# Kernel optimization log

Hardware: AMD Instinct MI355X
Metric: run time of the kernel (lower is better)

## Reference

```python
import jax, jax.numpy as jnp
import numpy as np

B, L, D, H = 8, 1024, 512, 8  # L must equal len_ for the skew trick
DH = D // H


def setup_inputs() -> dict:
    key = jax.random.key(0)
    ks = jax.random.split(key, 6)
    s = 0.02
    return {
        "x": jax.random.normal(ks[0], (B, L, D), dtype=jnp.float32),
        "Wq": jax.random.normal(ks[1], (D, D), dtype=jnp.float32) * s,
        "Wk": jax.random.normal(ks[2], (D, D), dtype=jnp.float32) * s,
        "Wv": jax.random.normal(ks[3], (D, D), dtype=jnp.float32) * s,
        "We": jax.random.normal(ks[4], (L, DH), dtype=jnp.float32) * s,  # e_projection weight: (len_, d_head)
        "Wo": jax.random.normal(ks[5], (D, D), dtype=jnp.float32) * s,
        "bo": jnp.zeros((D,), dtype=jnp.float32),
        "unused": 0,
    }


def reference(x, Wq, Wk, Wv, We, Wo, bo, unused):
    Bx, Lx, Dx = x.shape
    q = (x @ Wq.T).reshape(Bx, Lx, H, DH)  # blhd
    k = (x @ Wk.T).reshape(Bx, Lx, H, DH)
    v = (x @ Wv.T).reshape(Bx, Lx, H, DH)

    # relative-position logits: e_projection(q) then permute -> (B, H, L, len_)
    qe = jnp.einsum('blhd,ed->bhle', q, We)

    # 'skew' trick: reflect-pad right by L-1, zero-pad (right 1, bottom L-1),
    # reshape (B,H,2L-1,2L) -> (B,H,2L,2L-1), slice [:L, L-1:] -> (B,H,L,L)
    qe = jnp.pad(qe, ((0, 0), (0, 0), (0, 0), (0, Lx - 1)), mode='reflect')
    qe = jnp.pad(qe, ((0, 0), (0, 0), (0, Lx - 1), (0, 1)))
    qe = qe.reshape(Bx, H, 2 * Lx, 2 * Lx - 1)
    s_rel = qe[:, :, :Lx, Lx - 1:]

    scale = 1.0 / jnp.sqrt(jnp.asarray(DH, dtype=x.dtype))
    scores = jnp.einsum('blhd,bshd->bhls', q, k)
    A = jax.nn.softmax(scale * (scores + s_rel), axis=-1)
    V = jnp.einsum('bhls,bshd->blhd', A, v).reshape(Bx, Lx, Dx)
    return V @ Wo.T + bo
```

## Files before the change

### kernel.cpp

```cpp
#include <hip/hip_runtime.h>

#define Lc 1024
#define Dc 512
#define Hc 8
#define DHc 64

typedef __attribute__((ext_vector_type(8))) short bf16x8;
typedef __attribute__((ext_vector_type(4))) float f32x4;

typedef __attribute__((address_space(1))) const unsigned int guint;
typedef __attribute__((address_space(3))) unsigned int luint;

__device__ __forceinline__ void gload_lds16(const void* g, void* l) {
    __builtin_amdgcn_global_load_lds((guint*)g, (luint*)l, 16, 0, 0);
}

__device__ __forceinline__ unsigned short f2bf(float f) {
    unsigned u = __float_as_uint(f);
    u += 0x7fffu + ((u >> 16) & 1u);
    return (unsigned short)(u >> 16);
}
__device__ __forceinline__ unsigned pk2(float a, float b) {
    return (unsigned)f2bf(a) | ((unsigned)f2bf(b) << 16);
}
__device__ __forceinline__ unsigned pk2t(float a, float b) {
    return __builtin_amdgcn_perm(__float_as_uint(b), __float_as_uint(a), 0x07060302u);
}
__device__ __forceinline__ float bf2f(unsigned short s) { return __uint_as_float(((unsigned)s) << 16); }

__global__ void cvt_all_kernel(
    const float* __restrict__ x,  const float* __restrict__ Wq,
    const float* __restrict__ Wk, const float* __restrict__ Wv,
    const float* __restrict__ Wo, const float* __restrict__ We,
    unsigned short* __restrict__ xb,  unsigned short* __restrict__ wqb,
    unsigned short* __restrict__ wkb, unsigned short* __restrict__ wvb,
    unsigned short* __restrict__ wob, unsigned short* __restrict__ wet)
{
    int bid = blockIdx.x;
    const float* src; unsigned short* dst; size_t base;
    if      (bid < 4096) { src = x;  dst = xb;  base = (size_t)bid * 1024; }
    else if (bid < 4352) { src = Wq; dst = wqb; base = (size_t)(bid-4096) * 1024; }
    else if (bid < 4608) { src = Wk; dst = wkb; base = (size_t)(bid-4352) * 1024; }
    else if (bid < 4864) { src = Wv; dst = wvb; base = (size_t)(bid-4608) * 1024; }
    else if (bid < 5120) { src = Wo; dst = wob; base = (size_t)(bid-4864) * 1024; }
    else                 { src = We; dst = wet; base = (size_t)(bid-5120) * 1024; }
    size_t i = base + (size_t)threadIdx.x * 4;
    float4 a = *(const float4*)&src[i];
    *(uint2*)&dst[i] = make_uint2(pk2(a.x, a.y), pk2(a.z, a.w));
}

__global__ __launch_bounds__(256, 3) void proj_mfma_kernel(
    const unsigned short* __restrict__ xb,
    const unsigned short* __restrict__ wq, const unsigned short* __restrict__ wk,
    const unsigned short* __restrict__ wv,
    unsigned short* __restrict__ qo, unsigned short* __restrict__ ko,
    unsigned short* __restrict__ vtg, float qscale)
{
    const unsigned short* W;
    if (blockIdx.z == 0)      W = wq;
    else if (blockIdx.z == 1) W = wk;
    else                      W = wv;

    __shared__ unsigned short smem[128 * 136];
    unsigned short* As = smem;
    unsigned short* Bs = smem + 8192;

    const int t = threadIdx.x;
    const int lane = t & 63, w = t >> 6;
    const int lq = lane >> 4, ln = lane & 15;
    const int m0 = blockIdx.y * 128, n0 = blockIdx.x * 128;
    const int wm = (w & 1) * 64, wn = (w >> 1) * 64;
    const int srow = t >> 3;
    const int lsg  = ((t & 7) ^ ((t >> 3) & 7)) * 8;
    const int key  = ln & 7;

    f32x4 acc[4][4];
    #pragma unroll
    for (int i = 0; i < 4; i++)
        #pragma unroll
        for (int j = 0; j < 4; j++) acc[i][j] = (f32x4){0.f,0.f,0.f,0.f};

    for (int c0 = 0; c0 < 512; c0 += 64) {
        __syncthreads();
        #pragma unroll
        for (int g = 0; g < 4; g++) {
            gload_lds16(&xb[(size_t)(m0 + 32*g + srow) * 512 + c0 + lsg], &As[(32*g + srow)*64 + (t&7)*8]);
            gload_lds16(&W [(size_t)(n0 + 32*g + srow) * 512 + c0 + lsg], &Bs[(32*g + srow)*64 + (t&7)*8]);
        }
        __syncthreads();

        #pragma unroll
        for (int kk = 0; kk < 2; kk++) {
            bf16x8 af[4], bf[4];
            #pragma unroll
            for (int i = 0; i < 4; i++)
                af[i] = *(bf16x8*)&As[(wm + 16*i + ln)*64 + ((kk*4 + lq) ^ key)*8];
            #pragma unroll
            for (int j = 0; j < 4; j++)
                bf[j] = *(bf16x8*)&Bs[(wn + 16*j + ln)*64 + ((kk*4 + lq) ^ key)*8];
            #pragma unroll
            for (int i = 0; i < 4; i++)
                #pragma unroll
                for (int j = 0; j < 4; j++)
                    acc[i][j] = __builtin_amdgcn_mfma_f32_16x16x32_bf16(af[i], bf[j], acc[i][j], 0, 0, 0);
        }
    }

    if (blockIdx.z < 2) {
        unsigned short* out = (blockIdx.z == 0) ? qo : ko;
        const float osc = (blockIdx.z == 0) ? qscale : 1.0f;
        #pragma unroll
        for (int i = 0; i < 4; i++) {
            #pragma unroll
            for (int r = 0; r < 4; r++) {
                int m = m0 + wm + 16*i + 4*lq + r;
                int b = m >> 10, l = m & 1023;
                #pragma unroll
                for (int j = 0; j < 4; j++) {
                    int n = n0 + wn + 16*j + ln;
                    int h = n >> 6, dh = n & 63;
                    out[((size_t)((b*Hc + h)*Lc + l))*DHc + dh] = f2bf(acc[i][j][r] * osc);
                }
            }
        }
    } else {
        __syncthreads();
        unsigned short* Ts = smem;
        #pragma unroll
        for (int i = 0; i < 4; i++) {
            int mlb = wm + 16*i + 4*lq;
            #pragma unroll
            for (int j = 0; j < 4; j++) {
                int nl = wn + 16*j + ln;
                *(uint2*)&Ts[nl*136 + mlb] = make_uint2(pk2(acc[i][j][0], acc[i][j][1]),
                                                        pk2(acc[i][j][2], acc[i][j][3]));
            }
        }
        __syncthreads();
        const int b = m0 >> 10, l0m = m0 & 1023;
        const int nl = t >> 1, seg = (t & 1) * 64;
        const int ng = n0 + nl, h = ng >> 6, dh = ng & 63;
        unsigned short* dst = vtg + (((size_t)(b*Hc + h))*DHc + dh)*Lc + l0m + seg;
        #pragma unroll
        for (int u = 0; u < 8; u++)
            *(uint4*)&dst[8*u] = *(uint4*)&Ts[nl*136 + seg + 8*u];
    }
}

__global__ __launch_bounds__(256, 4) void out_mfma_kernel(
    const unsigned short* __restrict__ A, const unsigned short* __restrict__ W,
    const float* __restrict__ bias, float* __restrict__ out)
{
    __shared__ unsigned short As[64 * 64];
    __shared__ unsigned short Bs[64 * 64];

    const int t = threadIdx.x;
    const int lane = t & 63, w = t >> 6;
    const int lq = lane >> 4, ln = lane & 15;
    const int m0 = blockIdx.y * 64, n0 = blockIdx.x * 64;
    const int wm = (w & 1) * 32, wn = (w >> 1) * 32;
    const int srow = t >> 3;
    const int lsg  = ((t & 7) ^ ((t >> 3) & 7)) * 8;
    const int key  = ln & 7;

    f32x4 acc[2][2];
    #pragma unroll
    for (int i = 0; i < 2; i++)
        #pragma unroll
        for (int j = 0; j < 2; j++) acc[i][j] = (f32x4){0.f,0.f,0.f,0.f};

    for (int c0 = 0; c0 < 512; c0 += 64) {
        __syncthreads();
        #pragma unroll
        for (int g = 0; g < 2; g++) {
            gload_lds16(&A[(size_t)(m0 + 32*g + srow) * 512 + c0 + lsg], &As[(32*g + srow)*64 + (t&7)*8]);
            gload_lds16(&W[(size_t)(n0 + 32*g + srow) * 512 + c0 + lsg], &Bs[(32*g + srow)*64 + (t&7)*8]);
        }
        __syncthreads();

        #pragma unroll
        for (int kk = 0; kk < 2; kk++) {
            bf16x8 af[2], bf[2];
            #pragma unroll
            for (int i = 0; i < 2; i++)
                af[i] = *(bf16x8*)&As[(wm + 16*i + ln)*64 + ((kk*4 + lq) ^ key)*8];
            #pragma unroll
            for (int j = 0; j < 2; j++)
                bf[j] = *(bf16x8*)&Bs[(wn + 16*j + ln)*64 + ((kk*4 + lq) ^ key)*8];
            #pragma unroll
            for (int i = 0; i < 2; i++)
                #pragma unroll
                for (int j = 0; j < 2; j++)
                    acc[i][j] = __builtin_amdgcn_mfma_f32_16x16x32_bf16(af[i], bf[j], acc[i][j], 0, 0, 0);
        }
    }

    float bb[2];
    #pragma unroll
    for (int j = 0; j < 2; j++) bb[j] = bias[n0 + wn + 16*j + ln];

    #pragma unroll
    for (int i = 0; i < 2; i++) {
        #pragma unroll
        for (int r = 0; r < 4; r++) {
            int m = m0 + wm + 16*i + 4*lq + r;
            #pragma unroll
            for (int j = 0; j < 2; j++) {
                int n = n0 + wn + 16*j + ln;
                out[(size_t)m * Dc + n] = acc[i][j][r] + bb[j];
            }
        }
    }
}

__global__ __launch_bounds__(256, 4) void attn_v9_kernel(
    const unsigned short* __restrict__ q, const unsigned short* __restrict__ k,
    const unsigned short* __restrict__ vtg, const unsigned short* __restrict__ wet,
    unsigned short* __restrict__ attn)
{
    __shared__ unsigned short ksp [2 * 64 * 32];
    __shared__ unsigned short vtp [2 * 64 * 32];
    __shared__ unsigned short ps2 [64 * 64];
    __shared__ unsigned short qes [128 * 64];

    unsigned short* wesp = ps2;

    const int t    = threadIdx.x;
    const int lane = t & 63, w = t >> 6;
    const int lq   = lane >> 4, ln = lane & 15;
    const int si   = w >> 1;
    const int li   = w & 1;

    const int n   = blockIdx.x;
    const int xcd = n & 7, idx = n >> 3;
    const int bh  = xcd * 8 + (idx >> 4);
    const int l0  = (idx & 15) * 64;

    const unsigned short* qb  = q   + (size_t)bh * (Lc * DHc);
    const unsigned short* kb  = k   + (size_t)bh * (Lc * DHc);
    const unsigned short* vtb = vtg + (size_t)bh * (DHc * Lc);

    const int trow = t >> 2;
    const int sseg = ((t & 3) ^ ((t >> 4) & 3)) * 8;
    const int swz  = (ln >> 2) & 3;

    const bf16x8 onesf = {(short)0x3F80,(short)0x3F80,(short)0x3F80,(short)0x3F80,
                          (short)0x3F80,(short)0x3F80,(short)0x3F80,(short)0x3F80};

    bf16x8 qf[2][2];
    #pragma unroll
    for (int lt = 0; lt < 2; lt++)
        #pragma unroll
        for (int kk = 0; kk < 2; kk++)
            qf[lt][kk] = *(const bf16x8*)&qb[(size_t)(l0 + 32*li + 16*lt + ln)*64 + kk*32 + lq*8];

    const int pb0 = 15 - (l0 >> 6);
    gload_lds16(&wet[(size_t)(64*pb0 + trow)*64 +      sseg], &wesp[t*8]);
    gload_lds16(&wet[(size_t)(64*pb0 + trow)*64 + 32 + sseg], &wesp[2048 + t*8]);
    __syncthreads();
    {
        f32x4 qec[2][2];
        #pragma unroll
        for (int lt = 0; lt < 2; lt++)
            #pragma unroll
            for (int et = 0; et < 2; et++) qec[lt][et] = (f32x4){0.f,0.f,0.f,0.f};
        #pragma unroll
        for (int kk = 0; kk < 2; kk++)
            #pragma unroll
            for (int et = 0; et < 2; et++) {
                bf16x8 wf = *(bf16x8*)&wesp[kk*2048 + (16*(2*si+et) + ln)*32 + (lq ^ swz)*8];
                #pragma unroll
                for (int lt = 0; lt < 2; lt++)
                    qec[lt][et] = __builtin_amdgcn_mfma_f32_16x16x32_bf16(qf[lt][kk], wf, qec[lt][et], 0, 0, 0);
            }
        const int cb = (pb0 & 1) * 64;
        #pragma unroll
        for (int et = 0; et < 2; et++) {
            const int row = cb + 16*(2*si+et) + ln;
            #pragma unroll
            for (int lt = 0; lt < 2; lt++)
                *(uint2*)&qes[row*64 + ((32*li + 16*lt + 4*lq) ^ (ln << 2))] =
                    make_uint2(pk2(qec[lt][et][0], qec[lt][et][1]),
                               pk2(qec[lt][et][2], qec[lt][et][3]));
        }
    }

    f32x4 Lacc[2];
    f32x4 Ov[2][2];
    #pragma unroll
    for (int lt = 0; lt < 2; lt++) {
        Lacc[lt] = (f32x4){0.f,0.f,0.f,0.f};
        #pragma unroll
        for (int dt = 0; dt < 2; dt++) Ov[dt][lt] = (f32x4){0.f,0.f,0.f,0.f};
    }

    int pbOld = pb0 - 1;

    for (int s0 = 0; s0 < Lc; s0 += 64) {
        const int c0  = l0 - s0;
        const int ac0 = c0 < 0 ? -c0 : c0;
        const int pb  = (960 - ac0) >> 6;
        const int newp = (pb > pbOld) ? pb + 1 : pb;
        pbOld = pb;
        const int cb = (newp & 1) * 64;

        __syncthreads();
        gload_lds16(&kb [(size_t)(s0 + trow)*64 +      sseg], &ksp [t*8]);
        gload_lds16(&kb [(size_t)(s0 + trow)*64 + 32 + sseg], &ksp [2048 + t*8]);
        gload_lds16(&vtb[(size_t)trow*1024 + s0 +      sseg], &vtp [t*8]);
        gload_lds16(&vtb[(size_t)trow*1024 + s0 + 32 + sseg], &vtp [2048 + t*8]);
        gload_lds16(&wet[(size_t)(64*newp + trow)*64 +      sseg], &wesp[t*8]);
        gload_lds16(&wet[(size_t)(64*newp + trow)*64 + 32 + sseg], &wesp[2048 + t*8]);
        __syncthreads();

        {
            f32x4 qec[2][2];
            #pragma unroll
            for (int lt = 0; lt < 2; lt++)
                #pragma unroll
                for (int et = 0; et < 2; et++) qec[lt][et] = (f32x4){0.f,0.f,0.f,0.f};
            #pragma unroll
            for (int kk = 0; kk < 2; kk++)
                #pragma unroll
                for (int et = 0; et < 2; et++) {
                    bf16x8 wf = *(bf16x8*)&wesp[kk*2048 + (16*(2*si+et) + ln)*32 + (lq ^ swz)*8];
                    #pragma unroll
                    for (int lt = 0; lt < 2; lt++)
                        qec[lt][et] = __builtin_amdgcn_mfma_f32_16x16x32_bf16(qf[lt][kk], wf, qec[lt][et], 0, 0, 0);
                }
            #pragma unroll
            for (int et = 0; et < 2; et++) {
                const int row = cb + 16*(2*si+et) + ln;
                #pragma unroll
                for (int lt = 0; lt < 2; lt++)
                    *(uint2*)&qes[row*64 + ((32*li + 16*lt + 4*lq) ^ (ln << 2))] =
                        make_uint2(pk2(qec[lt][et][0], qec[lt][et][1]),
                                   pk2(qec[lt][et][2], qec[lt][et][3]));
            }
        }

        __syncthreads();

        f32x4 sc[2][2];
        #pragma unroll
        for (int st = 0; st < 2; st++)
            #pragma unroll
            for (int lt = 0; lt < 2; lt++) sc[st][lt] = (f32x4){0.f,0.f,0.f,0.f};
        #pragma unroll
        for (int kk = 0; kk < 2; kk++)
            #pragma unroll
            for (int st = 0; st < 2; st++) {
                bf16x8 kf = *(bf16x8*)&ksp[kk*2048 + (32*si + 16*st + ln)*32 + (lq ^ swz)*8];
                #pragma unroll
                for (int lt = 0; lt < 2; lt++)
                    sc[st][lt] = __builtin_amdgcn_mfma_f32_16x16x32_bf16(kf, qf[lt][kk], sc[st][lt], 0, 0, 0);
            }

        #pragma unroll
        for (int st = 0; st < 2; st++)
            #pragma unroll
            for (int lt = 0; lt < 2; lt++) {
                const int lloc = 32*li + 16*lt + ln;
                const int sb   = 32*si + 16*st + 4*lq;
                float p[4];
                #pragma unroll
                for (int r = 0; r < 4; r++) {
                    int d  = c0 + lloc - (sb + r);
                    int ad = d < 0 ? -d : d;
                    int m  = 1023 - ad;
                    float bias = bf2f(qes[(m & 127)*64 + (lloc ^ ((m & 15) << 2))]);
                    p[r] = __builtin_amdgcn_exp2f(sc[st][lt][r] + bias);
                }
                const int blk = (4*si + 2*st + (lq >> 1)) ^ (ln & 7);
                *(uint2*)&ps2[lloc*64 + blk*8 + (lq & 1)*4] =
                    make_uint2(pk2t(p[0], p[1]), pk2t(p[2], p[3]));
            }

        __syncthreads();

        #pragma unroll
        for (int kk = 0; kk < 2; kk++) {
            bf16x8 pf[2];
            #pragma unroll
            for (int lt = 0; lt < 2; lt++) {
                const int row = 32*li + 16*lt + ln;
                pf[lt] = *(bf16x8*)&ps2[row*64 + ((4*kk + lq) ^ (ln & 7))*8];
            }
            #pragma unroll
            for (int lt = 0; lt < 2; lt++)
                Lacc[lt] = __builtin_amdgcn_mfma_f32_16x16x32_bf16(onesf, pf[lt], Lacc[lt], 0, 0, 0);
            #pragma unroll
            for (int dt = 0; dt < 2; dt++) {
                bf16x8 vf = *(bf16x8*)&vtp[kk*2048 + (32*si + 16*dt + ln)*32 + (lq ^ swz)*8];
                #pragma unroll
                for (int lt = 0; lt < 2; lt++)
                    Ov[dt][lt] = __builtin_amdgcn_mfma_f32_16x16x32_bf16(vf, pf[lt], Ov[dt][lt], 0, 0, 0);
            }
        }
    }

    const int b = bh >> 3, h = bh & 7;
    #pragma unroll
    for (int lt = 0; lt < 2; lt++) {
        const float inv = 1.f / Lacc[lt][0];
        const int l = l0 + 32*li + 16*lt + ln;
        unsigned short* dst = &attn[((size_t)(b*Lc + l))*Dc + h*DHc];
        #pragma unroll
        for (int dt = 0; dt < 2; dt++) {
            const int dh = 32*si + 16*dt + 4*lq;
            *(uint2*)&dst[dh] = make_uint2(pk2(Ov[dt][lt][0]*inv, Ov[dt][lt][1]*inv),
                                           pk2(Ov[dt][lt][2]*inv, Ov[dt][lt][3]*inv));
        }
    }
}

extern "C" void kernel_launch(void* const* d_in, const int* in_sizes, int n_in,
                              void* d_out, int out_size, void* d_ws, size_t ws_size,
                              hipStream_t stream)
{
    (void)in_sizes; (void)n_in; (void)out_size; (void)ws_size;
    const float* x  = (const float*)d_in[0];
    const float* Wq = (const float*)d_in[1];
    const float* Wk = (const float*)d_in[2];
    const float* Wv = (const float*)d_in[3];
    const float* We = (const float*)d_in[4];
    const float* Wo = (const float*)d_in[5];
    const float* bo = (const float*)d_in[6];

    const size_t NT = (size_t)8 * Hc * Lc * DHc;
    unsigned short* qw  = (unsigned short*)d_ws;
    unsigned short* kw  = qw  + NT;
    unsigned short* vtg = kw  + NT;
    unsigned short* xbf = vtg + NT;
    unsigned short* awb = xbf + NT;
    unsigned short* wqb = awb + NT;
    unsigned short* wkb = wqb + 262144;
    unsigned short* wvb = wkb + 262144;
    unsigned short* wob = wvb + 262144;
    unsigned short* wet = wob + 262144;

    cvt_all_kernel<<<5184, 256, 0, stream>>>(x, Wq, Wk, Wv, Wo, We,
                                             xbf, wqb, wkb, wvb, wob, wet);
    proj_mfma_kernel<<<dim3(4, 64, 3), 256, 0, stream>>>(xbf, wqb, wkb, wvb,
                                                         qw, kw, vtg,
                                                         0.125f * 1.44269504089f);
    attn_v9_kernel<<<1024, 256, 0, stream>>>(qw, kw, vtg, wet, awb);
    out_mfma_kernel<<<dim3(8, 128), 256, 0, stream>>>(awb, wob, bo, (float*)d_out);
}
```

Baseline: 170.6 us.

## Prefetch We tiles into registers and read K directly from global

The attention kernel stops staging K and the We relative-position tile through LDS. K fragments are now loaded straight from global memory into registers. The We fragments for the next 64-column step are prefetched into a register double buffer (wA/wB) while the current step runs, through a two-iteration unrolled lambda body. This drops one barrier per iteration and the LDS aliasing of the We tile onto the P buffer, so global latency can overlap with compute. In exchange it adds VGPR pressure under the 256x4 launch bound, which risks spills, and it issues redundant global K loads across waves that share the same rows.

```diff
diff --git a/kernel.cpp b/kernel.cpp
--- a/kernel.cpp
+++ b/kernel.cpp
@@ -213,17 +213,14 @@
     }
 }
 
-__global__ __launch_bounds__(256, 4) void attn_v9_kernel(
+__global__ __launch_bounds__(256, 4) void attn_v10_kernel(
     const unsigned short* __restrict__ q, const unsigned short* __restrict__ k,
     const unsigned short* __restrict__ vtg, const unsigned short* __restrict__ wet,
     unsigned short* __restrict__ attn)
 {
-    __shared__ unsigned short ksp [2 * 64 * 32];
     __shared__ unsigned short vtp [2 * 64 * 32];
     __shared__ unsigned short ps2 [64 * 64];
     __shared__ unsigned short qes [128 * 64];
-
-    unsigned short* wesp = ps2;
 
     const int t    = threadIdx.x;
     const int lane = t & 63, w = t >> 6;
@@ -255,9 +252,18 @@
             qf[lt][kk] = *(const bf16x8*)&qb[(size_t)(l0 + 32*li + 16*lt + ln)*64 + kk*32 + lq*8];
 
     const int pb0 = 15 - (l0 >> 6);
-    gload_lds16(&wet[(size_t)(64*pb0 + trow)*64 +      sseg], &wesp[t*8]);
-    gload_lds16(&wet[(size_t)(64*pb0 + trow)*64 + 32 + sseg], &wesp[2048 + t*8]);
-    __syncthreads();
+
+    bf16x8 wA[2][2], wB[2][2];
+    bf16x8 wpre[2][2];
+    #pragma unroll
+    for (int kk = 0; kk < 2; kk++)
+        #pragma unroll
+        for (int et = 0; et < 2; et++) {
+            const size_t ro = (size_t)(16*(2*si+et) + ln)*64 + kk*32 + lq*8;
+            wpre[kk][et] = *(const bf16x8*)&wet[(size_t)(64*pb0    )*64 + ro];
+            wA  [kk][et] = *(const bf16x8*)&wet[(size_t)(64*(pb0+1))*64 + ro];
+        }
+
     {
         f32x4 qec[2][2];
         #pragma unroll
@@ -267,12 +273,10 @@
         #pragma unroll
         for (int kk = 0; kk < 2; kk++)
             #pragma unroll
-            for (int et = 0; et < 2; et++) {
-                bf16x8 wf = *(bf16x8*)&wesp[kk*2048 + (16*(2*si+et) + ln)*32 + (lq ^ swz)*8];
+            for (int et = 0; et < 2; et++)
                 #pragma unroll
                 for (int lt = 0; lt < 2; lt++)
-                    qec[lt][et] = __builtin_amdgcn_mfma_f32_16x16x32_bf16(qf[lt][kk], wf, qec[lt][et], 0, 0, 0);
-            }
+                    qec[lt][et] = __builtin_amdgcn_mfma_f32_16x16x32_bf16(qf[lt][kk], wpre[kk][et], qec[lt][et], 0, 0, 0);
         const int cb = (pb0 & 1) * 64;
         #pragma unroll
         for (int et = 0; et < 2; et++) {
@@ -296,7 +300,7 @@
 
     int pbOld = pb0 - 1;
 
-    for (int s0 = 0; s0 < Lc; s0 += 64) {
+    auto body = [&](int s0, bf16x8 (&wcur)[2][2], bf16x8 (&wnxt)[2][2]) {
         const int c0  = l0 - s0;
         const int ac0 = c0 < 0 ? -c0 : c0;
         const int pb  = (960 - ac0) >> 6;
@@ -304,14 +308,29 @@
         pbOld = pb;
         const int cb = (newp & 1) * 64;
 
-        __syncthreads();
-        gload_lds16(&kb [(size_t)(s0 + trow)*64 +      sseg], &ksp [t*8]);
-        gload_lds16(&kb [(size_t)(s0 + trow)*64 + 32 + sseg], &ksp [2048 + t*8]);
-        gload_lds16(&vtb[(size_t)trow*1024 + s0 +      sseg], &vtp [t*8]);
-        gload_lds16(&vtb[(size_t)trow*1024 + s0 + 32 + sseg], &vtp [2048 + t*8]);
-        gload_lds16(&wet[(size_t)(64*newp + trow)*64 +      sseg], &wesp[t*8]);
-        gload_lds16(&wet[(size_t)(64*newp + trow)*64 + 32 + sseg], &wesp[2048 + t*8]);
-        __syncthreads();
+        const int nc0  = c0 - 64;
+        const int nac0 = nc0 < 0 ? -nc0 : nc0;
+        int npb = (960 - nac0) >> 6;
+        int nnp = (npb > pb) ? npb + 1 : npb;
+        if (nnp < 0) nnp = 0;
+        const int ns0 = s0 + 64;
+
+        __syncthreads();
+
+        gload_lds16(&vtb[(size_t)trow*1024 + s0 +      sseg], &vtp[t*8]);
+        gload_lds16(&vtb[(size_t)trow*1024 + s0 + 32 + sseg], &vtp[2048 + t*8]);
+
+        bf16x8 kcur[2][2];
+        #pragma unroll
+        for (int kk = 0; kk < 2; kk++)
+            #pragma unroll
+            for (int st = 0; st < 2; st++)
+                kcur[kk][st] = *(const bf16x8*)&kb[(size_t)(ns0 - 64 + 32*si + 16*st + ln)*64 + kk*32 + lq*8];
+        #pragma unroll
+        for (int kk = 0; kk < 2; kk++)
+            #pragma unroll
+            for (int et = 0; et < 2; et++)
+                wnxt[kk][et] = *(const bf16x8*)&wet[(size_t)(64*nnp + 16*(2*si+et) + ln)*64 + kk*32 + lq*8];
 
         {
             f32x4 qec[2][2];
@@ -322,12 +341,10 @@
             #pragma unroll
             for (int kk = 0; kk < 2; kk++)
                 #pragma unroll
-                for (int et = 0; et < 2; et++) {
-                    bf16x8 wf = *(bf16x8*)&wesp[kk*2048 + (16*(2*si+et) + ln)*32 + (lq ^ swz)*8];
+                for (int et = 0; et < 2; et++)
                     #pragma unroll
                     for (int lt = 0; lt < 2; lt++)
-                        qec[lt][et] = __builtin_amdgcn_mfma_f32_16x16x32_bf16(qf[lt][kk], wf, qec[lt][et], 0, 0, 0);
-                }
+                        qec[lt][et] = __builtin_amdgcn_mfma_f32_16x16x32_bf16(qf[lt][kk], wcur[kk][et], qec[lt][et], 0, 0, 0);
             #pragma unroll
             for (int et = 0; et < 2; et++) {
                 const int row = cb + 16*(2*si+et) + ln;
@@ -349,12 +366,10 @@
         #pragma unroll
         for (int kk = 0; kk < 2; kk++)
             #pragma unroll
-            for (int st = 0; st < 2; st++) {
-                bf16x8 kf = *(bf16x8*)&ksp[kk*2048 + (32*si + 16*st + ln)*32 + (lq ^ swz)*8];
+            for (int st = 0; st < 2; st++)
                 #pragma unroll
                 for (int lt = 0; lt < 2; lt++)
-                    sc[st][lt] = __builtin_amdgcn_mfma_f32_16x16x32_bf16(kf, qf[lt][kk], sc[st][lt], 0, 0, 0);
-            }
+                    sc[st][lt] = __builtin_amdgcn_mfma_f32_16x16x32_bf16(kcur[kk][st], qf[lt][kk], sc[st][lt], 0, 0, 0);
 
         #pragma unroll
         for (int st = 0; st < 2; st++)
@@ -397,6 +412,12 @@
                     Ov[dt][lt] = __builtin_amdgcn_mfma_f32_16x16x32_bf16(vf, pf[lt], Ov[dt][lt], 0, 0, 0);
             }
         }
+    };
+
+    #pragma unroll 1
+    for (int s0 = 0; s0 < Lc; s0 += 128) {
+        body(s0,      wA, wB);
+        body(s0 + 64, wB, wA);
     }
 
     const int b = bh >> 3, h = bh & 7;
@@ -444,6 +465,6 @@
     proj_mfma_kernel<<<dim3(4, 64, 3), 256, 0, stream>>>(xbf, wqb, wkb, wvb,
                                                          qw, kw, vtg,
                                                          0.125f * 1.44269504089f);
-    attn_v9_kernel<<<1024, 256, 0, stream>>>(qw, kw, vtg, wet, awb);
+    attn_v10_kernel<<<1024, 256, 0, stream>>>(qw, kw, vtg, wet, awb);
     out_mfma_kernel<<<dim3(8, 128), 256, 0, stream>>>(awb, wob, bo, (float*)d_out);
 }
```

Result: slower. 188.7 us (+10.6%).

## Prefetch next K and relative-position weight tiles during attention compute phases

Applied to the files above, without the earlier changes.

Gives the We-tile a dedicated LDS buffer instead of aliasing it with the P buffer. The next iteration's We and K tiles are now issued asynchronously after the phases that consume the current ones, so their load latency overlaps the score and PV MFMA work. Only the V tile is still loaded at the top of each iteration. This adds LDS use, which may lower occupancy, and depends on the barrier placement being correct.

```diff
diff --git a/kernel.cpp b/kernel.cpp
--- a/kernel.cpp
+++ b/kernel.cpp
@@ -213,17 +213,16 @@
     }
 }
 
-__global__ __launch_bounds__(256, 4) void attn_v9_kernel(
+__global__ __launch_bounds__(256, 4) void attn_v11_kernel(
     const unsigned short* __restrict__ q, const unsigned short* __restrict__ k,
     const unsigned short* __restrict__ vtg, const unsigned short* __restrict__ wet,
     unsigned short* __restrict__ attn)
 {
     __shared__ unsigned short ksp [2 * 64 * 32];
     __shared__ unsigned short vtp [2 * 64 * 32];
+    __shared__ unsigned short wesp[2 * 64 * 32];
     __shared__ unsigned short ps2 [64 * 64];
     __shared__ unsigned short qes [128 * 64];
-
-    unsigned short* wesp = ps2;
 
     const int t    = threadIdx.x;
     const int lane = t & 63, w = t >> 6;
@@ -255,9 +254,15 @@
             qf[lt][kk] = *(const bf16x8*)&qb[(size_t)(l0 + 32*li + 16*lt + ln)*64 + kk*32 + lq*8];
 
     const int pb0 = 15 - (l0 >> 6);
-    gload_lds16(&wet[(size_t)(64*pb0 + trow)*64 +      sseg], &wesp[t*8]);
-    gload_lds16(&wet[(size_t)(64*pb0 + trow)*64 + 32 + sseg], &wesp[2048 + t*8]);
+
+    gload_lds16(&wet[(size_t)(64*pb0 + trow)*64 +      sseg], &ps2 [t*8]);
+    gload_lds16(&wet[(size_t)(64*pb0 + trow)*64 + 32 + sseg], &ps2 [2048 + t*8]);
+    gload_lds16(&wet[(size_t)(64*(pb0+1) + trow)*64 +      sseg], &wesp[t*8]);
+    gload_lds16(&wet[(size_t)(64*(pb0+1) + trow)*64 + 32 + sseg], &wesp[2048 + t*8]);
+    gload_lds16(&kb [(size_t)trow*64 +      sseg], &ksp [t*8]);
+    gload_lds16(&kb [(size_t)trow*64 + 32 + sseg], &ksp [2048 + t*8]);
     __syncthreads();
+
     {
         f32x4 qec[2][2];
         #pragma unroll
@@ -268,7 +273,7 @@
         for (int kk = 0; kk < 2; kk++)
             #pragma unroll
             for (int et = 0; et < 2; et++) {
-                bf16x8 wf = *(bf16x8*)&wesp[kk*2048 + (16*(2*si+et) + ln)*32 + (lq ^ swz)*8];
+                bf16x8 wf = *(bf16x8*)&ps2[kk*2048 + (16*(2*si+et) + ln)*32 + (lq ^ swz)*8];
                 #pragma unroll
                 for (int lt = 0; lt < 2; lt++)
                     qec[lt][et] = __builtin_amdgcn_mfma_f32_16x16x32_bf16(qf[lt][kk], wf, qec[lt][et], 0, 0, 0);
@@ -296,6 +301,7 @@
 
     int pbOld = pb0 - 1;
 
+    #pragma unroll 1
     for (int s0 = 0; s0 < Lc; s0 += 64) {
         const int c0  = l0 - s0;
         const int ac0 = c0 < 0 ? -c0 : c0;
@@ -303,15 +309,16 @@
         const int newp = (pb > pbOld) ? pb + 1 : pb;
         pbOld = pb;
         const int cb = (newp & 1) * 64;
-
-        __syncthreads();
-        gload_lds16(&kb [(size_t)(s0 + trow)*64 +      sseg], &ksp [t*8]);
-        gload_lds16(&kb [(size_t)(s0 + trow)*64 + 32 + sseg], &ksp [2048 + t*8]);
-        gload_lds16(&vtb[(size_t)trow*1024 + s0 +      sseg], &vtp [t*8]);
-        gload_lds16(&vtb[(size_t)trow*1024 + s0 + 32 + sseg], &vtp [2048 + t*8]);
-        gload_lds16(&wet[(size_t)(64*newp + trow)*64 +      sseg], &wesp[t*8]);
-        gload_lds16(&wet[(size_t)(64*newp + trow)*64 + 32 + sseg], &wesp[2048 + t*8]);
-        __syncthreads();
+        const bool more = (s0 < Lc - 64);
+        const int nc  = c0 - 64;
+        const int nac = nc < 0 ? -nc : nc;
+        const int npb = (960 - nac) >> 6;
+        const int nnp = (npb > pb) ? npb + 1 : npb;
+
+        __syncthreads();
+
+        gload_lds16(&vtb[(size_t)trow*1024 + s0 +      sseg], &vtp[t*8]);
+        gload_lds16(&vtb[(size_t)trow*1024 + s0 + 32 + sseg], &vtp[2048 + t*8]);
 
         {
             f32x4 qec[2][2];
@@ -340,6 +347,11 @@
         }
 
         __syncthreads();
+
+        if (more) {
+            gload_lds16(&wet[(size_t)(64*nnp + trow)*64 +      sseg], &wesp[t*8]);
+            gload_lds16(&wet[(size_t)(64*nnp + trow)*64 + 32 + sseg], &wesp[2048 + t*8]);
+        }
 
         f32x4 sc[2][2];
         #pragma unroll
@@ -377,6 +389,11 @@
             }
 
         __syncthreads();
+
+        if (more) {
+            gload_lds16(&kb[(size_t)(s0 + 64 + trow)*64 +      sseg], &ksp[t*8]);
+            gload_lds16(&kb[(size_t)(s0 + 64 + trow)*64 + 32 + sseg], &ksp[2048 + t*8]);
+        }
 
         #pragma unroll
         for (int kk = 0; kk < 2; kk++) {
@@ -444,6 +461,6 @@
     proj_mfma_kernel<<<dim3(4, 64, 3), 256, 0, stream>>>(xbf, wqb, wkb, wvb,
                                                          qw, kw, vtg,
                                                          0.125f * 1.44269504089f);
-    attn_v9_kernel<<<1024, 256, 0, stream>>>(qw, kw, vtg, wet, awb);
+    attn_v11_kernel<<<1024, 256, 0, stream>>>(qw, kw, vtg, wet, awb);
     out_mfma_kernel<<<dim3(8, 128), 256, 0, stream>>>(awb, wob, bo, (float*)d_out);
 }
```

Measured after the change: 173.4 us. No clear change (+1.7%).
